# Kernel tuning notes

Hardware: AMD Instinct MI355X
Metric: run time of the kernel (lower is better)

The kernel has to match this reference:

```python
import jax, jax.numpy as jnp
import numpy as np
import math

GROUP = 64
DIM = 4096


def _hadamard(group):
    # normalized Hadamard matrix via Sylvester construction, matching constructH
    H = np.ones((1, 1), dtype=np.float32)
    for _ in range(int(math.log2(group))):
        H = np.block([[H, H], [H, -H]]) / math.sqrt(2)
    return jnp.asarray(H)


def setup_inputs() -> dict:
    key = jax.random.key(0)
    x = jax.random.normal(key, (4, 4096, DIM), dtype=jnp.float32)
    # learnable parameter: Hadamard block repeated dim//group times -> [dim/group, group, group]
    H = jnp.broadcast_to(_hadamard(GROUP), (DIM // GROUP, GROUP, GROUP)).copy()
    return {"x": x, "H": H}


def reference(x, H):
    # x: [..., dim] -> view tokens as [N, dim/group, group], apply per-block matmul by H
    x_shape = x.shape
    n_blocks, group = H.shape[0], H.shape[1]
    xb = x.reshape(-1, n_blocks, group)            # [N, G, g]
    yb = jnp.einsum('ngk,gkh->ngh', xb, H)          # block-diagonal transform
    return yb.reshape(x_shape)
```

## Files before the change

kernel.cpp:

```cpp
#include <hip/hip_runtime.h>
#include <hip/hip_bf16.h>


#define DIM 4096
#define NG   64
#define GSZ  64
#define TOK_PER_BLK 256

typedef __bf16 bf16x8 __attribute__((ext_vector_type(8)));
typedef float  f32x4  __attribute__((ext_vector_type(4)));

__global__ __launch_bounds__(256, 4)
void hh_mfma_kernel(const float* __restrict__ x, const float* __restrict__ H,
                    float* __restrict__ y, int ntok) {
    __shared__ __align__(16) float Hl[GSZ * GSZ];

    const int g    = blockIdx.x & (NG - 1);
    const int tb   = blockIdx.x >> 6;
    const int tid  = threadIdx.x;
    const int lane = tid & 63;
    const int wave = tid >> 6;

    const float* __restrict__ Hg = H + (size_t)g * (GSZ * GSZ);
    #pragma unroll
    for (int i = 0; i < 4; ++i) {
        int idx = tid + i * 256;
        ((f32x4*)Hl)[idx] = ((const f32x4*)Hg)[idx];
    }
    __syncthreads();

    const int bcol = lane & 15;
    const int brow = (lane >> 4) * 8;
    bf16x8 bfrag[2][4];
    #pragma unroll
    for (int kt = 0; kt < 2; ++kt)
        #pragma unroll
        for (int ht = 0; ht < 4; ++ht)
            #pragma unroll
            for (int i = 0; i < 8; ++i)
                bfrag[kt][ht][i] =
                    (__bf16)Hl[(kt * 32 + brow + i) * GSZ + ht * 16 + bcol];

    const int arow  = lane & 15;
    const int acolk = (lane >> 4) * 8;
    const int crow0 = (lane >> 4) * 4;
    const int ccol  = lane & 15;

    const int tok0 = tb * TOK_PER_BLK + wave * 64;

    #pragma unroll
    for (int tt = 0; tt < 4; ++tt) {
        const int tbase = tok0 + tt * 16;

        bf16x8 afrag[2];
        const float* __restrict__ xp =
            x + (size_t)(tbase + arow) * DIM + g * GSZ + acolk;
        #pragma unroll
        for (int kt = 0; kt < 2; ++kt) {
            f32x4 lo = *(const f32x4*)(xp + kt * 32);
            f32x4 hi = *(const f32x4*)(xp + kt * 32 + 4);
            #pragma unroll
            for (int i = 0; i < 4; ++i) {
                afrag[kt][i]     = (__bf16)lo[i];
                afrag[kt][i + 4] = (__bf16)hi[i];
            }
        }

        f32x4 acc[4];
        #pragma unroll
        for (int ht = 0; ht < 4; ++ht) {
            acc[ht] = (f32x4){0.f, 0.f, 0.f, 0.f};
            acc[ht] = __builtin_amdgcn_mfma_f32_16x16x32_bf16(
                          afrag[0], bfrag[0][ht], acc[ht], 0, 0, 0);
            acc[ht] = __builtin_amdgcn_mfma_f32_16x16x32_bf16(
                          afrag[1], bfrag[1][ht], acc[ht], 0, 0, 0);
        }

        float* __restrict__ yp =
            y + (size_t)(tbase + crow0) * DIM + g * GSZ + ccol;
        #pragma unroll
        for (int ht = 0; ht < 4; ++ht)
            #pragma unroll
            for (int j = 0; j < 4; ++j)
                yp[(size_t)j * DIM + ht * 16] = acc[ht][j];
    }
}

extern "C" void kernel_launch(void* const* d_in, const int* in_sizes, int n_in,
                              void* d_out, int out_size, void* d_ws, size_t ws_size,
                              hipStream_t stream) {
    const float* x = (const float*)d_in[0];
    const float* H = (const float*)d_in[1];
    float* y = (float*)d_out;

    const int ntok = in_sizes[0] / DIM;
    const int nblk = (ntok / TOK_PER_BLK) * NG;

    hipLaunchKernelGGL(hh_mfma_kernel, dim3(nblk), dim3(256), 0, stream,
                       x, H, y, ntok);
}
```

Baseline: 120.9 us.

## Swap MFMA operands to compute transposed tile and store float4 nontemporally

Swaps the MFMA A and B operands so the kernel computes the transposed output tile. Each lane then holds four consecutive output columns for one token, so each output tile is written with a single 16-byte nontemporal vector store instead of four scattered scalar stores. The launch-bounds occupancy hint is also raised from 4 to 8 blocks per CU. Correctness depends on the transposed accumulator layout matching the new indexing, and the higher occupancy target may put pressure on registers.

Result: faster. 99.84 us (-17.4%).

```diff
diff --git a/kernel.cpp b/kernel.cpp
--- a/kernel.cpp
+++ b/kernel.cpp
@@ -10,7 +10,7 @@
 typedef __bf16 bf16x8 __attribute__((ext_vector_type(8)));
 typedef float  f32x4  __attribute__((ext_vector_type(4)));
 
-__global__ __launch_bounds__(256, 4)
+__global__ __launch_bounds__(256, 8)
 void hh_mfma_kernel(const float* __restrict__ x, const float* __restrict__ H,
                     float* __restrict__ y, int ntok) {
     __shared__ __align__(16) float Hl[GSZ * GSZ];
@@ -29,22 +29,21 @@
     }
     __syncthreads();
 
-    const int bcol = lane & 15;
-    const int brow = (lane >> 4) * 8;
-    bf16x8 bfrag[2][4];
+    const int hcol = lane & 15;
+    const int hrow = (lane >> 4) * 8;
+    bf16x8 hfrag[2][4];
     #pragma unroll
     for (int kt = 0; kt < 2; ++kt)
         #pragma unroll
         for (int ht = 0; ht < 4; ++ht)
             #pragma unroll
             for (int i = 0; i < 8; ++i)
-                bfrag[kt][ht][i] =
-                    (__bf16)Hl[(kt * 32 + brow + i) * GSZ + ht * 16 + bcol];
+                hfrag[kt][ht][i] =
+                    (__bf16)Hl[(kt * 32 + hrow + i) * GSZ + ht * 16 + hcol];
 
-    const int arow  = lane & 15;
+    const int tokl  = lane & 15;
     const int acolk = (lane >> 4) * 8;
-    const int crow0 = (lane >> 4) * 4;
-    const int ccol  = lane & 15;
+    const int hq    = (lane >> 4) * 4;
 
     const int tok0 = tb * TOK_PER_BLK + wave * 64;
 
@@ -52,17 +51,17 @@
     for (int tt = 0; tt < 4; ++tt) {
         const int tbase = tok0 + tt * 16;
 
-        bf16x8 afrag[2];
+        bf16x8 xfrag[2];
         const float* __restrict__ xp =
-            x + (size_t)(tbase + arow) * DIM + g * GSZ + acolk;
+            x + (size_t)(tbase + tokl) * DIM + g * GSZ + acolk;
         #pragma unroll
         for (int kt = 0; kt < 2; ++kt) {
             f32x4 lo = *(const f32x4*)(xp + kt * 32);
             f32x4 hi = *(const f32x4*)(xp + kt * 32 + 4);
             #pragma unroll
             for (int i = 0; i < 4; ++i) {
-                afrag[kt][i]     = (__bf16)lo[i];
-                afrag[kt][i + 4] = (__bf16)hi[i];
+                xfrag[kt][i]     = (__bf16)lo[i];
+                xfrag[kt][i + 4] = (__bf16)hi[i];
             }
         }
 
@@ -71,18 +70,16 @@
         for (int ht = 0; ht < 4; ++ht) {
             acc[ht] = (f32x4){0.f, 0.f, 0.f, 0.f};
             acc[ht] = __builtin_amdgcn_mfma_f32_16x16x32_bf16(
-                          afrag[0], bfrag[0][ht], acc[ht], 0, 0, 0);
+                          hfrag[0][ht], xfrag[0], acc[ht], 0, 0, 0);
             acc[ht] = __builtin_amdgcn_mfma_f32_16x16x32_bf16(
-                          afrag[1], bfrag[1][ht], acc[ht], 0, 0, 0);
+                          hfrag[1][ht], xfrag[1], acc[ht], 0, 0, 0);
         }
 
         float* __restrict__ yp =
-            y + (size_t)(tbase + crow0) * DIM + g * GSZ + ccol;
+            y + (size_t)(tbase + tokl) * DIM + g * GSZ + hq;
         #pragma unroll
         for (int ht = 0; ht < 4; ++ht)
-            #pragma unroll
-            for (int j = 0; j < 4; ++j)
-                yp[(size_t)j * DIM + ht * 16] = acc[ht][j];
+            __builtin_nontemporal_store(acc[ht], (f32x4*)(yp + ht * 16));
     }
 }
 
```
